# Performance work log

Measured on AMD Instinct MI355X. Metric: run time of the kernel, lower is better.

## Reference

```python
import jax, jax.numpy as jnp
import numpy as np
import math

D = 256      # d_model == channels
H = 8        # nhead
DEP = D // H # depth = 32
FF = 1024    # dim_feedforward
P = 81       # 9x9 shogi board tokens
EPS = 1e-5


def setup_inputs() -> dict:
    key = jax.random.key(0)
    ks = jax.random.split(key, 8)
    B = 2048
    x = jax.random.normal(ks[0], (B, D, 9, 9), dtype=jnp.float32)
    s = 0.02
    return {
        "x": x,
        "qkv_w": jax.random.normal(ks[1], (3 * D, D // H), dtype=jnp.float32) * s,  # grouped 1x1 conv weight
        "rel_w1": jax.random.normal(ks[2], (32, D * P), dtype=jnp.float32) * s,
        "rel_w2": jax.random.normal(ks[3], (DEP * P, 32), dtype=jnp.float32) * s,
        "o_w": jax.random.normal(ks[4], (D, D), dtype=jnp.float32) * s,
        "ff_w1": jax.random.normal(ks[5], (FF, D), dtype=jnp.float32) * s,
        "ff_w2": jax.random.normal(ks[6], (D, FF), dtype=jnp.float32) * s,
        "bn1_g": jnp.ones((D,), jnp.float32),
        "bn1_b": jnp.zeros((D,), jnp.float32),
        "bn2_g": jnp.ones((D,), jnp.float32),
        "bn2_b": jnp.zeros((D,), jnp.float32),
    }


def _batchnorm(x, g, b):
    # training-mode BN: per-channel batch stats over (B, H, W), biased variance
    mean = jnp.mean(x, axis=(0, 2, 3), keepdims=True)
    var = jnp.var(x, axis=(0, 2, 3), keepdims=True)
    return (x - mean) * jax.lax.rsqrt(var + EPS) * g[None, :, None, None] + b[None, :, None, None]


def reference(x, qkv_w, rel_w1, rel_w2, o_w, ff_w1, ff_w2, bn1_g, bn1_b, bn2_g, bn2_b):
    B = x.shape[0]
    # grouped 1x1 conv QKV: group g maps its D//H input channels to 3*DEP outputs
    xg = x.reshape(B, H, D // H, P)                      # [B, H, D/H, 81]
    wg = qkv_w.reshape(H, 3 * DEP, D // H)               # [H, 3*DEP, D/H]
    qkv = jnp.einsum('goi,bgip->bgop', wg, xg).reshape(B, 3 * D, P)
    q = qkv[:, :D].reshape(B, H, DEP, P).transpose(0, 1, 3, 2)       # [B,H,81,DEP]
    k = qkv[:, D:2 * D].reshape(B, H, DEP, P)                        # [B,H,DEP,81]
    v = qkv[:, 2 * D:].reshape(B, H, DEP, P).transpose(0, 1, 3, 2)   # [B,H,81,DEP]
    # learned relative-position bias from the whole board state
    r = (x.reshape(B, -1) @ rel_w1.T) @ rel_w2.T          # [B, DEP*81]
    r = r.reshape(B, 1, DEP, P)                           # broadcast over heads
    scores = (q @ k + q @ r) / math.sqrt(DEP)             # [B,H,81,81]
    aw = jax.nn.softmax(scores, axis=-1)
    att = (aw @ v).transpose(0, 1, 3, 2).reshape(B, D, 9, 9)
    att = jnp.einsum('oc,bchw->bohw', o_w, att)           # 1x1 output projection
    x1 = _batchnorm(att + x, bn1_g, bn1_b)
    ff = jax.nn.gelu(jnp.einsum('fc,bchw->bfhw', ff_w1, x1), approximate=False)
    ff = jnp.einsum('cf,bfhw->bchw', ff_w2, ff)
    return _batchnorm(ff + x1, bn2_g, bn2_b)
```

## Files before the change

### kernel.cpp

```cpp
#include <hip/hip_runtime.h>
#include <math.h>

#define B_   2048
#define D_   256
#define H_   8
#define DEP_ 32
#define P_   81
#define FF_  1024
#define CHW  (D_*P_)
#define NPOS (B_*P_)
#define KREL (D_*P_)
#define NTOT (B_*CHW)
#define EPS_ 1e-5f
#define YTP  264
#define YTSZ (96*YTP)

typedef __attribute__((ext_vector_type(8))) short short8v;
typedef __attribute__((ext_vector_type(4))) short short4v;
typedef __attribute__((ext_vector_type(4))) float f32x4;

__device__ __forceinline__ float bf2f(unsigned short u){
    return __uint_as_float(((unsigned int)u) << 16);
}
__device__ __forceinline__ unsigned short f2bf(float f){
    unsigned int x = __float_as_uint(f);
    return (unsigned short)((x + 0x7FFFu + ((x >> 16) & 1u)) >> 16);
}
__device__ __forceinline__ float fast_gelu(float x){
    float s = __builtin_amdgcn_rcpf(1.f + __expf(-1.702f * x));
    return x * s;
}
__device__ __forceinline__ float wave16_red(float v){
    v += __shfl_xor(v, 1); v += __shfl_xor(v, 2);
    v += __shfl_xor(v, 4); v += __shfl_xor(v, 8);
    return v;
}
__device__ __forceinline__ short8v frag_redist(const f32x4 c0, const f32x4 c1, int lr, int lh){
    short8v o;
    #pragma unroll
    for (int j = 0; j < 8; ++j){
        int src = lr + 16 * (2 * (lh & 1) + (j >> 2));
        float v0 = __shfl(c0[j & 3], src);
        float v1 = __shfl(c1[j & 3], src);
        o[j] = (short)f2bf(lh < 2 ? v0 : v1);
    }
    return o;
}

__global__ __launch_bounds__(256) void k_f2bf(const float* __restrict__ w,
                                              unsigned short* __restrict__ o, int n){
    int i = blockIdx.x * 256 + threadIdx.x;
    int st = gridDim.x * 256;
    for (; i < n; i += st) o[i] = f2bf(w[i]);
}

__global__ __launch_bounds__(256) void k_h_mfma(const float* __restrict__ x,
                                                const unsigned short* __restrict__ w1b,
                                                float* __restrict__ ph){
    const int bt = blockIdx.x >> 2, ks = blockIdx.x & 3;
    const int t = threadIdx.x, w = t >> 6, lane = t & 63;
    const int lr = lane & 15, lh = lane >> 4;
    const int b0 = bt * 16;
    f32x4 acc0 = {0.f,0.f,0.f,0.f}, acc1 = {0.f,0.f,0.f,0.f};
    const float* xrow = x + (size_t)(b0 + lr) * KREL;
    const unsigned short* wr0 = w1b + (size_t)lr * KREL;
    const unsigned short* wr1 = w1b + (size_t)(16 + lr) * KREL;
    for (int kk = w; kk < 162; kk += 4){
        const int k0 = (ks * 162 + kk) * 32 + lh * 8;
        short8v a0 = *(const short8v*)(wr0 + k0);
        short8v a1 = *(const short8v*)(wr1 + k0);
        const float4 xv0 = *(const float4*)(xrow + k0);
        const float4 xv1 = *(const float4*)(xrow + k0 + 4);
        short8v bb;
        bb[0] = (short)f2bf(xv0.x); bb[1] = (short)f2bf(xv0.y);
        bb[2] = (short)f2bf(xv0.z); bb[3] = (short)f2bf(xv0.w);
        bb[4] = (short)f2bf(xv1.x); bb[5] = (short)f2bf(xv1.y);
        bb[6] = (short)f2bf(xv1.z); bb[7] = (short)f2bf(xv1.w);
        acc0 = __builtin_amdgcn_mfma_f32_16x16x32_bf16(a0, bb, acc0, 0, 0, 0);
        acc1 = __builtin_amdgcn_mfma_f32_16x16x32_bf16(a1, bb, acc1, 0, 0, 0);
    }
    __shared__ float red[4][32][17];
    #pragma unroll
    for (int r = 0; r < 4; ++r){
        red[w][lh * 4 + r][lr]      = acc0[r];
        red[w][16 + lh * 4 + r][lr] = acc1[r];
    }
    __syncthreads();
    for (int i = t; i < 512; i += 256){
        int j = i >> 4, bb2 = i & 15;
        float s = red[0][j][bb2] + red[1][j][bb2] + red[2][j][bb2] + red[3][j][bb2];
        ph[(size_t)ks * 65536 + (size_t)(b0 + bb2) * 32 + j] = s;
    }
}

__global__ __launch_bounds__(256) void k_h_red(const float* __restrict__ ph,
                                               float* __restrict__ h){
    int i = blockIdx.x * 256 + threadIdx.x;
    h[i] = ph[i] + ph[65536 + i] + ph[131072 + i] + ph[196608 + i];
}

__global__ __launch_bounds__(512, 2) void k_attn_oproj8(const float* __restrict__ x,
                                                        const unsigned short* __restrict__ qkvwb,
                                                        const float* __restrict__ relw2,
                                                        const float* __restrict__ h,
                                                        const unsigned short* __restrict__ owb,
                                                        unsigned short* __restrict__ yT,
                                                        float* __restrict__ p1){
    const int b = blockIdx.x, t = threadIdx.x;
    const int lane = t & 63, w = t >> 6;
    const int lr = lane & 15, lh = lane >> 4;

    __shared__ __align__(16) unsigned short x1s[96 * 264];
    __shared__ __align__(16) unsigned short Rl[96 * 40];
    __shared__ __align__(16) unsigned short vL[8][32 * 104];
    __shared__ __align__(16) unsigned short pL[8][16 * 104];
    unsigned short* attT = (unsigned short*)vL;

    const float* xb = x + (size_t)b * CHW;

    {
        const float* hb = h + b * 32;
        float hreg[32];
        #pragma unroll
        for (int j = 0; j < 32; ++j) hreg[j] = hb[j];
        for (int idx = t; idx < 2592; idx += 512){
            int d = idx / 81, p = idx - d * 81;
            const float4* wr = (const float4*)(relw2 + (size_t)idx * 32);
            float s = 0.f;
            #pragma unroll
            for (int j = 0; j < 8; ++j){
                float4 wv = wr[j];
                s += wv.x * hreg[4*j] + wv.y * hreg[4*j+1] + wv.z * hreg[4*j+2] + wv.w * hreg[4*j+3];
            }
            Rl[p * 40 + d] = f2bf(s);
        }
        for (int idx = t; idx < 15 * 32; idx += 512){
            int p = 81 + (idx >> 5), d = idx & 31;
            Rl[p * 40 + d] = 0;
        }
    }
    for (int idx = t; idx < 15 * 132; idx += 512){
        int r = idx / 132, c = idx - r * 132;
        *(unsigned int*)&x1s[(81 + r) * 264 + 2 * c] = 0;
    }
    {
        float* tb = (float*)vL;
        for (int cc = 0; cc < 4; ++cc){
            for (int idx = t; idx < 64 * 81; idx += 512){
                int c = idx / 81, p = idx - c * 81;
                tb[c * 85 + p] = xb[(cc * 64 + c) * 81 + p];
            }
            __syncthreads();
            for (int idx = t; idx < 32 * 81; idx += 512){
                int c2 = idx & 31, p = idx >> 5;
                int c = 2 * c2;
                unsigned int pk = (unsigned int)f2bf(tb[c * 85 + p])
                                | ((unsigned int)f2bf(tb[(c + 1) * 85 + p]) << 16);
                *(unsigned int*)&x1s[p * 264 + cc * 64 + c] = pk;
            }
            __syncthreads();
        }
    }

    const int hh = w;
    const int qrow = hh * 32, krow = 256 + hh * 32, vrow = 512 + hh * 32;
    const int gq = (qrow / 96) * 32, gk = (krow / 96) * 32, gv = (vrow / 96) * 32;
    unsigned short* v_ = vL[w];
    unsigned short* p_ = pL[w];

    short8v bqf[6];
    {
        short8v a0 = *(const short8v*)(qkvwb + (size_t)(qrow + lr) * 32 + lh * 8);
        short8v a1 = *(const short8v*)(qkvwb + (size_t)(qrow + 16 + lr) * 32 + lh * 8);
        #pragma unroll
        for (int nt = 0; nt < 6; ++nt){
            short8v bb = *(const short8v*)(x1s + (nt * 16 + lr) * 264 + gq + lh * 8);
            f32x4 c0 = {0.f,0.f,0.f,0.f}, c1 = {0.f,0.f,0.f,0.f};
            c0 = __builtin_amdgcn_mfma_f32_16x16x32_bf16(a0, bb, c0, 0, 0, 0);
            c1 = __builtin_amdgcn_mfma_f32_16x16x32_bf16(a1, bb, c1, 0, 0, 0);
            bqf[nt] = frag_redist(c0, c1, lr, lh);
        }
    }
    short8v akf[6];
    {
        short8v a0 = *(const short8v*)(qkvwb + (size_t)(krow + lr) * 32 + lh * 8);
        short8v a1 = *(const short8v*)(qkvwb + (size_t)(krow + 16 + lr) * 32 + lh * 8);
        #pragma unroll
        for (int mt = 0; mt < 6; ++mt){
            int p = mt * 16 + lr;
            short4v r0 = *(const short4v*)(Rl + p * 40 + lh * 4);
            short4v r1 = *(const short4v*)(Rl + p * 40 + 16 + lh * 4);
            f32x4 c0, c1;
            #pragma unroll
            for (int r = 0; r < 4; ++r){
                c0[r] = bf2f((unsigned short)r0[r]);
                c1[r] = bf2f((unsigned short)r1[r]);
            }
            short8v bb = *(const short8v*)(x1s + p * 264 + gk + lh * 8);
            c0 = __builtin_amdgcn_mfma_f32_16x16x32_bf16(a0, bb, c0, 0, 0, 0);
            c1 = __builtin_amdgcn_mfma_f32_16x16x32_bf16(a1, bb, c1, 0, 0, 0);
            akf[mt] = frag_redist(c0, c1, lr, lh);
        }
    }
    {
        short8v a0 = *(const short8v*)(qkvwb + (size_t)(vrow + lr) * 32 + lh * 8);
        short8v a1 = *(const short8v*)(qkvwb + (size_t)(vrow + 16 + lr) * 32 + lh * 8);
        #pragma unroll
        for (int nt = 0; nt < 6; ++nt){
            short8v bb = *(const short8v*)(x1s + (nt * 16 + lr) * 264 + gv + lh * 8);
            f32x4 c0 = {0.f,0.f,0.f,0.f}, c1 = {0.f,0.f,0.f,0.f};
            c0 = __builtin_amdgcn_mfma_f32_16x16x32_bf16(a0, bb, c0, 0, 0, 0);
            c1 = __builtin_amdgcn_mfma_f32_16x16x32_bf16(a1, bb, c1, 0, 0, 0);
            int pk = nt * 16 + lr;
            #pragma unroll
            for (int r = 0; r < 4; ++r){
                v_[(lh * 4 + r) * 104 + pk]      = f2bf(c0[r]);
                v_[(16 + lh * 4 + r) * 104 + pk] = f2bf(c1[r]);
            }
        }
    }

    f32x4 oA[6], oB[6];
    #pragma unroll
    for (int nt = 0; nt < 6; ++nt){
        f32x4 sc[6];
        #pragma unroll
        for (int mt = 0; mt < 6; ++mt){
            f32x4 z = {0.f,0.f,0.f,0.f};
            sc[mt] = __builtin_amdgcn_mfma_f32_16x16x32_bf16(akf[mt], bqf[nt], z, 0, 0, 0);
        }
        sc[5][0] = (lh == 0) ? sc[5][0] : -1e30f;
        sc[5][1] = -1e30f; sc[5][2] = -1e30f; sc[5][3] = -1e30f;
        float mx = -1e30f;
        #pragma unroll
        for (int mt = 0; mt < 6; ++mt)
        #pragma unroll
        for (int r = 0; r < 4; ++r) mx = fmaxf(mx, sc[mt][r]);
        mx = fmaxf(mx, __shfl_xor(mx, 16));
        mx = fmaxf(mx, __shfl_xor(mx, 32));
        const float scl = 0.17677669529663687f;
        float sum = 0.f;
        #pragma unroll
        for (int mt = 0; mt < 6; ++mt)
        #pragma unroll
        for (int r = 0; r < 4; ++r){
            float e = __expf((sc[mt][r] - mx) * scl);
            sc[mt][r] = e; sum += e;
        }
        sum += __shfl_xor(sum, 16);
        sum += __shfl_xor(sum, 32);
        float inv = 1.f / sum;
        #pragma unroll
        for (int mt = 0; mt < 6; ++mt){
            short4v pv;
            #pragma unroll
            for (int r = 0; r < 4; ++r) pv[r] = (short)f2bf(sc[mt][r] * inv);
            *(short4v*)(p_ + lr * 104 + mt * 16 + lh * 4) = pv;
        }
        f32x4 o0 = {0.f,0.f,0.f,0.f}, o1 = {0.f,0.f,0.f,0.f};
        #pragma unroll
        for (int ks = 0; ks < 3; ++ks){
            short8v ap  = *(const short8v*)(p_ + lr * 104 + ks * 32 + lh * 8);
            short8v bv0 = *(const short8v*)(v_ + lr * 104 + ks * 32 + lh * 8);
            short8v bv1 = *(const short8v*)(v_ + (16 + lr) * 104 + ks * 32 + lh * 8);
            o0 = __builtin_amdgcn_mfma_f32_16x16x32_bf16(ap, bv0, o0, 0, 0, 0);
            o1 = __builtin_amdgcn_mfma_f32_16x16x32_bf16(ap, bv1, o1, 0, 0, 0);
        }
        oA[nt] = o0;
        oB[nt] = o1;
    }

    __syncthreads();
    #pragma unroll
    for (int nt = 0; nt < 6; ++nt){
        #pragma unroll
        for (int r = 0; r < 4; ++r){
            int pq = nt * 16 + lh * 4 + r;
            if (pq < 81){
                attT[pq * 264 + hh * 32 + lr]      = f2bf(oA[nt][r]);
                attT[pq * 264 + hh * 32 + 16 + lr] = f2bf(oB[nt][r]);
            } else {
                attT[pq * 264 + hh * 32 + lr]      = 0;
                attT[pq * 264 + hh * 32 + 16 + lr] = 0;
            }
        }
    }
    __syncthreads();

    const int cw = w * 32;
    f32x4 acc[2][6];
    #pragma unroll
    for (int ci = 0; ci < 2; ++ci)
    #pragma unroll
    for (int pj = 0; pj < 6; ++pj)
        acc[ci][pj] = (f32x4){0.f, 0.f, 0.f, 0.f};

    for (int ks = 0; ks < 8; ++ks){
        const int k0 = ks * 32 + lh * 8;
        short8v a[2];
        #pragma unroll
        for (int ci = 0; ci < 2; ++ci)
            a[ci] = *(const short8v*)(owb + (size_t)(cw + ci * 16 + lr) * 256 + k0);
        #pragma unroll
        for (int pj = 0; pj < 6; ++pj){
            short8v bb = *(const short8v*)(attT + (pj * 16 + lr) * 264 + k0);
            #pragma unroll
            for (int ci = 0; ci < 2; ++ci)
                acc[ci][pj] = __builtin_amdgcn_mfma_f32_16x16x32_bf16(a[ci], bb, acc[ci][pj], 0, 0, 0);
        }
    }
    unsigned short* yb = yT + (size_t)b * YTSZ;
    float cs[8], cq[8];
    #pragma unroll
    for (int i = 0; i < 8; ++i){ cs[i] = 0.f; cq[i] = 0.f; }
    #pragma unroll
    for (int ci = 0; ci < 2; ++ci)
    #pragma unroll
    for (int pj = 0; pj < 6; ++pj){
        int p = pj * 16 + lr;
        int c = cw + ci * 16 + lh * 4;
        short4v pk;
        if (p < 81){
            short4v xv = *(const short4v*)&x1s[p * 264 + c];
            #pragma unroll
            for (int r = 0; r < 4; ++r){
                float y = acc[ci][pj][r] + bf2f((unsigned short)xv[r]);
                pk[r] = (short)f2bf(y);
                cs[ci * 4 + r] += y;
                cq[ci * 4 + r] += y * y;
            }
        } else {
            #pragma unroll
            for (int r = 0; r < 4; ++r) pk[r] = 0;
        }
        *(short4v*)(yb + p * YTP + c) = pk;
    }
    #pragma unroll
    for (int i = 0; i < 8; ++i){
        cs[i] = wave16_red(cs[i]);
        cq[i] = wave16_red(cq[i]);
    }
    if (lr == 0){
        #pragma unroll
        for (int ci = 0; ci < 2; ++ci)
        #pragma unroll
        for (int r = 0; r < 4; ++r){
            int c = cw + ci * 16 + lh * 4 + r;
            p1[(size_t)c * 2048 + b]         = cs[ci * 4 + r];
            p1[(size_t)(256 + c) * 2048 + b] = cq[ci * 4 + r];
        }
    }
}

__global__ __launch_bounds__(256) void k_red(const float* __restrict__ part,
                                             const float* __restrict__ g, const float* __restrict__ bia,
                                             float* __restrict__ sOut, float* __restrict__ tOut){
    const int c = blockIdx.x, t = threadIdx.x;
    float s = 0.f, q = 0.f;
    #pragma unroll
    for (int i = 0; i < 8; ++i){
        s += part[(size_t)c * 2048 + t + i * 256];
        q += part[(size_t)(256 + c) * 2048 + t + i * 256];
    }
    __shared__ float rs[256], rq[256];
    rs[t] = s; rq[t] = q;
    __syncthreads();
    for (int k = 128; k; k >>= 1){
        if (t < k){ rs[t] += rs[t + k]; rq[t] += rq[t + k]; }
        __syncthreads();
    }
    if (t == 0){
        float m = rs[0] / (float)NPOS;
        float var = rq[0] / (float)NPOS - m * m;
        float sc = g[c] * rsqrtf(var + EPS_);
        sOut[c] = sc;
        tOut[c] = bia[c] - m * sc;
    }
}

__global__ __launch_bounds__(256) void k_w1scale(const float* __restrict__ w1,
                                                 const float* __restrict__ s1,
                                                 unsigned short* __restrict__ w1s){
    const int f = blockIdx.x, t = threadIdx.x;
    w1s[f * 256 + t] = f2bf(w1[f * 256 + t] * s1[t]);
}

__global__ __launch_bounds__(64) void k_bias1(const float* __restrict__ w1,
                                              const float* __restrict__ t1,
                                              float* __restrict__ bias1){
    const int f = blockIdx.x, t = threadIdx.x;
    const float4 wv = *(const float4*)(w1 + f * 256 + t * 4);
    const float4 tv = *(const float4*)(t1 + t * 4);
    float s = wv.x * tv.x + wv.y * tv.y + wv.z * tv.z + wv.w * tv.w;
    #pragma unroll
    for (int m = 1; m < 64; m <<= 1) s += __shfl_xor(s, m);
    if (t == 0) bias1[f] = s;
}

__global__ __launch_bounds__(256, 2) void k_ff_v4(unsigned short* __restrict__ yT,
                                                  const unsigned short* __restrict__ w1s,
                                                  const unsigned short* __restrict__ w2bf,
                                                  const float* __restrict__ bias1,
                                                  const float* __restrict__ s1, const float* __restrict__ t1,
                                                  float* __restrict__ p2){
    const int b = blockIdx.x, t = threadIdx.x;
    const int lane = t & 63, w = t >> 6;
    const int lr = lane & 15, lh = lane >> 4;

    __shared__ __align__(16) unsigned short x1s[96 * 264];
    __shared__ __align__(16) unsigned short ffs[2][96 * 72];

    {
        const short8v* src = (const short8v*)(yT + (size_t)b * YTSZ);
        short8v* dst = (short8v*)x1s;
        for (int idx = t; idx < 3168; idx += 256) dst[idx] = src[idx];
    }
    __syncthreads();

    const int cw = w * 64;
    const int fl = w * 16 + lh * 4;
    f32x4 acc2[4][6];
    #pragma unroll
    for (int ci = 0; ci < 4; ++ci)
    #pragma unroll
    for (int pj = 0; pj < 6; ++pj)
        acc2[ci][pj] = (f32x4){0.f, 0.f, 0.f, 0.f};

    auto g1_kloop = [&](int fc, f32x4 (&acc1)[6]){
        const int fbase = fc * 64 + w * 16;
        float b4[4];
        #pragma unroll
        for (int r = 0; r < 4; ++r) b4[r] = bias1[fbase + lh * 4 + r];
        #pragma unroll
        for (int pj = 0; pj < 6; ++pj){
            acc1[pj][0] = b4[0]; acc1[pj][1] = b4[1];
            acc1[pj][2] = b4[2]; acc1[pj][3] = b4[3];
        }
        #pragma unroll
        for (int ks = 0; ks < 8; ++ks){
            const int k0 = ks * 32 + lh * 8;
            short8v a0 = *(const short8v*)(w1s + (size_t)(fbase + lr) * 256 + k0);
            #pragma unroll
            for (int pj = 0; pj < 6; ++pj){
                short8v bb = *(const short8v*)(x1s + (pj * 16 + lr) * 264 + k0);
                acc1[pj] = __builtin_amdgcn_mfma_f32_16x16x32_bf16(a0, bb, acc1[pj], 0, 0, 0);
            }
        }
    };
    auto g2 = [&](int fc, int bf){
        #pragma unroll
        for (int ks2 = 0; ks2 < 2; ++ks2){
            const int k0 = ks2 * 32 + lh * 8;
            short8v a2[4];
            #pragma unroll
            for (int ci = 0; ci < 4; ++ci)
                a2[ci] = *(const short8v*)(w2bf + (size_t)(cw + ci * 16 + lr) * 1024 + fc * 64 + k0);
            #pragma unroll
            for (int pj = 0; pj < 6; ++pj){
                short8v bb = *(const short8v*)(ffs[bf] + (pj * 16 + lr) * 72 + k0);
                #pragma unroll
                for (int ci = 0; ci < 4; ++ci)
                    acc2[ci][pj] = __builtin_amdgcn_mfma_f32_16x16x32_bf16(a2[ci], bb, acc2[ci][pj], 0, 0, 0);
            }
        }
    };
    auto gelu_store = [&](const f32x4 (&acc1)[6], int bf){
        #pragma unroll
        for (int pj = 0; pj < 6; ++pj){
            int p = pj * 16 + lr;
            short4v pk;
            #pragma unroll
            for (int r = 0; r < 4; ++r)
                pk[r] = (short)f2bf(fast_gelu(acc1[pj][r]));
            *(short4v*)&ffs[bf][p * 72 + fl] = pk;
        }
    };

    {
        f32x4 acc1[6];
        g1_kloop(0, acc1);
        gelu_store(acc1, 0);
    }
    __syncthreads();
    for (int fc = 0; fc < 15; ++fc){
        f32x4 acc1[6];
        g1_kloop(fc + 1, acc1);
        g2(fc, fc & 1);
        gelu_store(acc1, (fc + 1) & 1);
        __syncthreads();
    }
    g2(15, 1);

    float sv[16], tv[16];
    #pragma unroll
    for (int ci = 0; ci < 4; ++ci)
    #pragma unroll
    for (int r = 0; r < 4; ++r){
        int c = cw + ci * 16 + lh * 4 + r;
        sv[ci * 4 + r] = s1[c];
        tv[ci * 4 + r] = t1[c];
    }
    unsigned short* zb = yT + (size_t)b * YTSZ;
    float cs[16], cq[16];
    #pragma unroll
    for (int i = 0; i < 16; ++i){ cs[i] = 0.f; cq[i] = 0.f; }
    #pragma unroll
    for (int ci = 0; ci < 4; ++ci)
    #pragma unroll
    for (int pj = 0; pj < 6; ++pj){
        int p = pj * 16 + lr;
        if (p < 81){
            int c = cw + ci * 16 + lh * 4;
            short4v yv = *(const short4v*)&x1s[p * 264 + c];
            short4v pk;
            #pragma unroll
            for (int r = 0; r < 4; ++r){
                float x1 = fmaf(bf2f((unsigned short)yv[r]), sv[ci * 4 + r], tv[ci * 4 + r]);
                float z = acc2[ci][pj][r] + x1;
                pk[r] = (short)f2bf(z);
                cs[ci * 4 + r] += z;
                cq[ci * 4 + r] += z * z;
            }
            *(short4v*)(zb + p * YTP + c) = pk;
        }
    }
    #pragma unroll
    for (int i = 0; i < 16; ++i){
        cs[i] = wave16_red(cs[i]);
        cq[i] = wave16_red(cq[i]);
    }
    if (lr == 0){
        #pragma unroll
        for (int ci = 0; ci < 4; ++ci)
        #pragma unroll
        for (int r = 0; r < 4; ++r){
            int c = cw + ci * 16 + lh * 4 + r;
            p2[(size_t)c * 2048 + b]         = cs[ci * 4 + r];
            p2[(size_t)(256 + c) * 2048 + b] = cq[ci * 4 + r];
        }
    }
}

__global__ __launch_bounds__(256) void k_bnapply_t(const unsigned short* __restrict__ yTz,
                                                   const float* __restrict__ s2, const float* __restrict__ t2,
                                                   float* __restrict__ out){
    const int b = blockIdx.x, t = threadIdx.x;
    __shared__ __align__(16) unsigned short zs[96 * 264];
    __shared__ float s2s[256], t2s[256];
    s2s[t] = s2[t];
    t2s[t] = t2[t];
    {
        const short8v* src = (const short8v*)(yTz + (size_t)b * YTSZ);
        short8v* dst = (short8v*)zs;
        for (int idx = t; idx < 3168; idx += 256) dst[idx] = src[idx];
    }
    __syncthreads();
    float* ob = out + (size_t)b * CHW;
    for (int idx = t; idx < CHW; idx += 256){
        int c = idx / 81, p = idx - c * 81;
        ob[idx] = fmaf(bf2f(zs[p * 264 + c]), s2s[c], t2s[c]);
    }
}

extern "C" void kernel_launch(void* const* d_in, const int* in_sizes, int n_in,
                              void* d_out, int out_size, void* d_ws, size_t ws_size,
                              hipStream_t stream){
    const float* x     = (const float*)d_in[0];
    const float* qkvw  = (const float*)d_in[1];
    const float* relw1 = (const float*)d_in[2];
    const float* relw2 = (const float*)d_in[3];
    const float* ow    = (const float*)d_in[4];
    const float* ffw1  = (const float*)d_in[5];
    const float* ffw2  = (const float*)d_in[6];
    const float* g1    = (const float*)d_in[7];
    const float* b1    = (const float*)d_in[8];
    const float* g2    = (const float*)d_in[9];
    const float* b2    = (const float*)d_in[10];
    float* out = (float*)d_out;
    char* ws = (char*)d_ws;

    unsigned short* w1rel = (unsigned short*)ws;
    float* h     = (float*)(ws + 1327104);
    unsigned short* w2bf  = (unsigned short*)(ws + 2117632);
    unsigned short* qkvwb = (unsigned short*)(ws + 2641920);
    unsigned short* owb   = (unsigned short*)(ws + 2691072);
    unsigned short* w1s   = (unsigned short*)(ws + 2822144);
    float* bias1 = (float*)(ws + 3346432);
    float* s1    = (float*)(ws + 3350528);
    float* t1    = (float*)(ws + 3351552);
    float* s2    = (float*)(ws + 3352576);
    float* t2    = (float*)(ws + 3353600);
    float* p1    = (float*)(ws + 3354624);
    float* p2    = (float*)(ws + 7548928);
    unsigned short* yT = (unsigned short*)(ws + 11743232);
    float* p_h = p1;

    hipLaunchKernelGGL(k_f2bf, dim3(1024), dim3(256), 0, stream, relw1, w1rel, 663552);
    hipLaunchKernelGGL(k_f2bf, dim3(256),  dim3(256), 0, stream, ffw2, w2bf, 262144);
    hipLaunchKernelGGL(k_f2bf, dim3(96),   dim3(256), 0, stream, qkvw, qkvwb, 24576);
    hipLaunchKernelGGL(k_f2bf, dim3(256),  dim3(256), 0, stream, ow, owb, 65536);

    hipLaunchKernelGGL(k_h_mfma, dim3(512), dim3(256), 0, stream, x, w1rel, p_h);
    hipLaunchKernelGGL(k_h_red,  dim3(256), dim3(256), 0, stream, p_h, h);
    hipLaunchKernelGGL(k_attn_oproj8, dim3(2048), dim3(512), 0, stream, x, qkvwb, relw2, h, owb, yT, p1);
    hipLaunchKernelGGL(k_red,      dim3(256),  dim3(256), 0, stream, p1, g1, b1, s1, t1);
    hipLaunchKernelGGL(k_w1scale,  dim3(1024), dim3(256), 0, stream, ffw1, s1, w1s);
    hipLaunchKernelGGL(k_bias1,    dim3(1024), dim3(64),  0, stream, ffw1, t1, bias1);
    hipLaunchKernelGGL(k_ff_v4,    dim3(2048), dim3(256), 0, stream, yT, w1s, w2bf, bias1, s1, t1, p2);
    hipLaunchKernelGGL(k_red,      dim3(256),  dim3(256), 0, stream, p2, g2, b2, s2, t2);
    hipLaunchKernelGGL(k_bnapply_t, dim3(2048), dim3(256), 0, stream, yT, s2, t2, out);
}
```

Baseline: 793.6 us.

## Merge prep kernels, simplify x transpose, add MFMA priority hints

Four weight-conversion launches become one k_prep kernel, and the w1 scaling and bias kernels become one k_w1prep kernel, cutting launch overhead and a second read of ff_w1. The attention kernel now loads x directly into the bf16 transposed LDS tile in one pass instead of four staged chunks with barriers, at the cost of strided global reads. s_setprio hints are placed around the MFMA loops to favour matrix-issuing waves.

```diff
diff --git a/kernel.cpp b/kernel.cpp
--- a/kernel.cpp
+++ b/kernel.cpp
@@ -47,11 +47,22 @@
     return o;
 }
 
-__global__ __launch_bounds__(256) void k_f2bf(const float* __restrict__ w,
-                                              unsigned short* __restrict__ o, int n){
+__global__ __launch_bounds__(256) void k_prep(const float* __restrict__ relw1,
+                                              const float* __restrict__ ffw2,
+                                              const float* __restrict__ qkvw,
+                                              const float* __restrict__ ow,
+                                              unsigned short* __restrict__ w1rel,
+                                              unsigned short* __restrict__ w2bf,
+                                              unsigned short* __restrict__ qkvwb,
+                                              unsigned short* __restrict__ owb){
     int i = blockIdx.x * 256 + threadIdx.x;
     int st = gridDim.x * 256;
-    for (; i < n; i += st) o[i] = f2bf(w[i]);
+    for (; i < 1015808; i += st){
+        if (i < 663552)                w1rel[i]           = f2bf(relw1[i]);
+        else if (i < 925696)           w2bf[i - 663552]   = f2bf(ffw2[i - 663552]);
+        else if (i < 950272)           qkvwb[i - 925696]  = f2bf(qkvw[i - 925696]);
+        else                           owb[i - 950272]    = f2bf(ow[i - 950272]);
+    }
 }
 
 __global__ __launch_bounds__(256) void k_h_mfma(const float* __restrict__ x,
@@ -143,24 +154,14 @@
         int r = idx / 132, c = idx - r * 132;
         *(unsigned int*)&x1s[(81 + r) * 264 + 2 * c] = 0;
     }
-    {
-        float* tb = (float*)vL;
-        for (int cc = 0; cc < 4; ++cc){
-            for (int idx = t; idx < 64 * 81; idx += 512){
-                int c = idx / 81, p = idx - c * 81;
-                tb[c * 85 + p] = xb[(cc * 64 + c) * 81 + p];
-            }
-            __syncthreads();
-            for (int idx = t; idx < 32 * 81; idx += 512){
-                int c2 = idx & 31, p = idx >> 5;
-                int c = 2 * c2;
-                unsigned int pk = (unsigned int)f2bf(tb[c * 85 + p])
-                                | ((unsigned int)f2bf(tb[(c + 1) * 85 + p]) << 16);
-                *(unsigned int*)&x1s[p * 264 + cc * 64 + c] = pk;
-            }
-            __syncthreads();
-        }
-    }
+    for (int idx = t; idx < 81 * 128; idx += 512){
+        int c2 = idx / 81, p = idx - c2 * 81;
+        int c = 2 * c2;
+        unsigned int pk = (unsigned int)f2bf(xb[c * 81 + p])
+                        | ((unsigned int)f2bf(xb[(c + 1) * 81 + p]) << 16);
+        *(unsigned int*)&x1s[p * 264 + c] = pk;
+    }
+    __syncthreads();
 
     const int hh = w;
     const int qrow = hh * 32, krow = 256 + hh * 32, vrow = 512 + hh * 32;
@@ -168,6 +169,7 @@
     unsigned short* v_ = vL[w];
     unsigned short* p_ = pL[w];
 
+    __builtin_amdgcn_s_setprio(1);
     short8v bqf[6];
     {
         short8v a0 = *(const short8v*)(qkvwb + (size_t)(qrow + lr) * 32 + lh * 8);
@@ -269,6 +271,7 @@
         oA[nt] = o0;
         oB[nt] = o1;
     }
+    __builtin_amdgcn_s_setprio(0);
 
     __syncthreads();
     #pragma unroll
@@ -295,6 +298,7 @@
     for (int pj = 0; pj < 6; ++pj)
         acc[ci][pj] = (f32x4){0.f, 0.f, 0.f, 0.f};
 
+    __builtin_amdgcn_s_setprio(1);
     for (int ks = 0; ks < 8; ++ks){
         const int k0 = ks * 32 + lh * 8;
         short8v a[2];
@@ -309,6 +313,7 @@
                 acc[ci][pj] = __builtin_amdgcn_mfma_f32_16x16x32_bf16(a[ci], bb, acc[ci][pj], 0, 0, 0);
         }
     }
+    __builtin_amdgcn_s_setprio(0);
     unsigned short* yb = yT + (size_t)b * YTSZ;
     float cs[8], cq[8];
     #pragma unroll
@@ -378,23 +383,21 @@
     }
 }
 
-__global__ __launch_bounds__(256) void k_w1scale(const float* __restrict__ w1,
-                                                 const float* __restrict__ s1,
-                                                 unsigned short* __restrict__ w1s){
+__global__ __launch_bounds__(256) void k_w1prep(const float* __restrict__ w1,
+                                                const float* __restrict__ s1v,
+                                                const float* __restrict__ t1v,
+                                                unsigned short* __restrict__ w1s,
+                                                float* __restrict__ bias1){
     const int f = blockIdx.x, t = threadIdx.x;
-    w1s[f * 256 + t] = f2bf(w1[f * 256 + t] * s1[t]);
-}
-
-__global__ __launch_bounds__(64) void k_bias1(const float* __restrict__ w1,
-                                              const float* __restrict__ t1,
-                                              float* __restrict__ bias1){
-    const int f = blockIdx.x, t = threadIdx.x;
-    const float4 wv = *(const float4*)(w1 + f * 256 + t * 4);
-    const float4 tv = *(const float4*)(t1 + t * 4);
-    float s = wv.x * tv.x + wv.y * tv.y + wv.z * tv.z + wv.w * tv.w;
+    float wv = w1[f * 256 + t];
+    w1s[f * 256 + t] = f2bf(wv * s1v[t]);
+    float s = wv * t1v[t];
     #pragma unroll
     for (int m = 1; m < 64; m <<= 1) s += __shfl_xor(s, m);
-    if (t == 0) bias1[f] = s;
+    __shared__ float red[4];
+    if ((t & 63) == 0) red[t >> 6] = s;
+    __syncthreads();
+    if (t == 0) bias1[f] = red[0] + red[1] + red[2] + red[3];
 }
 
 __global__ __launch_bounds__(256, 2) void k_ff_v4(unsigned short* __restrict__ yT,
@@ -436,6 +439,7 @@
             acc1[pj][0] = b4[0]; acc1[pj][1] = b4[1];
             acc1[pj][2] = b4[2]; acc1[pj][3] = b4[3];
         }
+        __builtin_amdgcn_s_setprio(1);
         #pragma unroll
         for (int ks = 0; ks < 8; ++ks){
             const int k0 = ks * 32 + lh * 8;
@@ -446,8 +450,10 @@
                 acc1[pj] = __builtin_amdgcn_mfma_f32_16x16x32_bf16(a0, bb, acc1[pj], 0, 0, 0);
             }
         }
+        __builtin_amdgcn_s_setprio(0);
     };
     auto g2 = [&](int fc, int bf){
+        __builtin_amdgcn_s_setprio(1);
         #pragma unroll
         for (int ks2 = 0; ks2 < 2; ++ks2){
             const int k0 = ks2 * 32 + lh * 8;
@@ -463,6 +469,7 @@
                     acc2[ci][pj] = __builtin_amdgcn_mfma_f32_16x16x32_bf16(a2[ci], bb, acc2[ci][pj], 0, 0, 0);
             }
         }
+        __builtin_amdgcn_s_setprio(0);
     };
     auto gelu_store = [&](const f32x4 (&acc1)[6], int bf){
         #pragma unroll
@@ -595,18 +602,14 @@
     unsigned short* yT = (unsigned short*)(ws + 11743232);
     float* p_h = p1;
 
-    hipLaunchKernelGGL(k_f2bf, dim3(1024), dim3(256), 0, stream, relw1, w1rel, 663552);
-    hipLaunchKernelGGL(k_f2bf, dim3(256),  dim3(256), 0, stream, ffw2, w2bf, 262144);
-    hipLaunchKernelGGL(k_f2bf, dim3(96),   dim3(256), 0, stream, qkvw, qkvwb, 24576);
-    hipLaunchKernelGGL(k_f2bf, dim3(256),  dim3(256), 0, stream, ow, owb, 65536);
-
+    hipLaunchKernelGGL(k_prep, dim3(1024), dim3(256), 0, stream,
+                       relw1, ffw2, qkvw, ow, w1rel, w2bf, qkvwb, owb);
     hipLaunchKernelGGL(k_h_mfma, dim3(512), dim3(256), 0, stream, x, w1rel, p_h);
     hipLaunchKernelGGL(k_h_red,  dim3(256), dim3(256), 0, stream, p_h, h);
     hipLaunchKernelGGL(k_attn_oproj8, dim3(2048), dim3(512), 0, stream, x, qkvwb, relw2, h, owb, yT, p1);
-    hipLaunchKernelGGL(k_red,      dim3(256),  dim3(256), 0, stream, p1, g1, b1, s1, t1);
-    hipLaunchKernelGGL(k_w1scale,  dim3(1024), dim3(256), 0, stream, ffw1, s1, w1s);
-    hipLaunchKernelGGL(k_bias1,    dim3(1024), dim3(64),  0, stream, ffw1, t1, bias1);
-    hipLaunchKernelGGL(k_ff_v4,    dim3(2048), dim3(256), 0, stream, yT, w1s, w2bf, bias1, s1, t1, p2);
-    hipLaunchKernelGGL(k_red,      dim3(256),  dim3(256), 0, stream, p2, g2, b2, s2, t2);
+    hipLaunchKernelGGL(k_red,     dim3(256),  dim3(256), 0, stream, p1, g1, b1, s1, t1);
+    hipLaunchKernelGGL(k_w1prep,  dim3(1024), dim3(256), 0, stream, ffw1, s1, t1, w1s, bias1);
+    hipLaunchKernelGGL(k_ff_v4,   dim3(2048), dim3(256), 0, stream, yT, w1s, w2bf, bias1, s1, t1, p2);
+    hipLaunchKernelGGL(k_red,     dim3(256),  dim3(256), 0, stream, p2, g2, b2, s2, t2);
     hipLaunchKernelGGL(k_bnapply_t, dim3(2048), dim3(256), 0, stream, yT, s2, t2, out);
 }
```

Measured after the change: 690.8 us. -13.0%, faster.
